# Kernel tuning notes

Measured on AMD Instinct MI355X. Metric: run time of the kernel, lower is better.

## Reference

```python
import jax, jax.numpy as jnp
import numpy as np

PROJ = 8192     # projDim
THRESH = 1e-8   # numerical-stability epsilon for signed sqrt
L2_EPS = 1e-12  # eps of torch F.normalize


def setup_inputs() -> dict:
    key = jax.random.key(0)
    k1, k2, k3, k4, k5 = jax.random.split(key, 5)
    B, C, H, W = 16, 512, 14, 14
    x = jax.random.normal(k1, (B, C, H, W), dtype=jnp.float32)
    h1 = jax.random.randint(k2, (C,), 0, PROJ, dtype=jnp.int32)
    h2 = jax.random.randint(k3, (C,), 0, PROJ, dtype=jnp.int32)
    s1 = (2 * jax.random.randint(k4, (C,), 0, 2) - 1).astype(jnp.float32)
    s2 = (2 * jax.random.randint(k5, (C,), 0, 2) - 1).astype(jnp.float32)
    return {"x": x, "s1": s1, "s2": s2, "h1": h1, "h2": h2}


def reference(x, s1, s2, h1, h2):
    # x: [B, C, H, W]; h*: [C] hash buckets in [0, PROJ); s*: [C] signs (+-1)
    B, C, H, W = x.shape
    x_flat = jnp.transpose(x, (0, 2, 3, 1)).reshape(-1, C)  # [N, C], N = B*H*W

    def count_sketch(s, h):
        # Equivalent to x_flat @ M with M[c, h[c]] = s[c]: scatter-add of
        # sign-weighted channels into PROJ bins.  -> [N, PROJ]
        return jax.ops.segment_sum((x_flat * s).T, h, num_segments=PROJ).T

    fft1 = jnp.fft.fft(count_sketch(s1, h1), axis=-1)
    fft2 = jnp.fft.fft(count_sketch(s2, h2), axis=-1)
    conv = jnp.fft.ifft(fft1 * fft2, axis=-1).real       # [N, PROJ]
    y = conv.reshape(B, H, W, PROJ).sum(axis=(1, 2))      # sum pool -> [B, PROJ]
    y = jnp.sign(y) * jnp.sqrt(jnp.abs(y) + THRESH)       # signed sqrt
    norm = jnp.linalg.norm(y, axis=1, keepdims=True)
    return y / jnp.maximum(norm, L2_EPS)                  # l2 normalize (dim=1)
```

## Files before the change

### kernel.cpp

```cpp
#include <hip/hip_runtime.h>
#include <math.h>

#define PROJ 8192
#define NB   16
#define NC   512
#define HW   196
#define NKC  7
#define LST  40

typedef __attribute__((ext_vector_type(8))) short bf16x8;
typedef __attribute__((ext_vector_type(4))) short short4v;
typedef __attribute__((ext_vector_type(4))) float f32x4;

__device__ __forceinline__ unsigned bf16_rne(float f) {
    unsigned u = __builtin_bit_cast(unsigned, f);
    return (u + 0x7fffu + ((u >> 16) & 1u)) >> 16;
}

__global__ __launch_bounds__(1024, 4)
void cbp_gram_mfma(const float* __restrict__ x,
                   const float* __restrict__ s1,
                   const float* __restrict__ s2,
                   const int*   __restrict__ h1,
                   const int*   __restrict__ h2,
                   float* __restrict__ gsk) {
    __shared__ float sk[PROJ];
    __shared__ short Ah[128 * LST];
    __shared__ short Al[128 * LST];
    __shared__ short Bh[128 * LST];
    __shared__ short Bl[128 * LST];
    __shared__ int   lh1[128], lh2[128];
    __shared__ float lsA[128], lsB[128];

    const int tid = threadIdx.x;
    const int blk = blockIdx.x;
    const int b    = 2 * (blk & 7) + (blk >> 7);
    const int tile = (blk >> 3) & 15;
    const int I = tile >> 2, J = tile & 3;
    const int c1base = I * 128;
    const int c2base = J * 128;

    const int lane = tid & 63;
    const int wave = tid >> 6;
    const int quad = lane >> 4;
    const int l15  = lane & 15;
    const int wr   = (wave >> 2) * 32;
    const int wc   = (wave & 3) * 32;

    for (int i = tid; i < PROJ; i += 1024) sk[i] = 0.f;
    if (tid < 128) {
        lh1[tid] = h1[c1base + tid];  lsA[tid] = s1[c1base + tid];
        lh2[tid] = h2[c2base + tid];  lsB[tid] = s2[c2base + tid];
    }

    const float* xa = x + ((size_t)b * NC + c1base) * HW;
    const float* xb = x + ((size_t)b * NC + c2base) * HW;

    f32x4 acc[2][2];
#pragma unroll
    for (int i = 0; i < 2; ++i)
#pragma unroll
        for (int j = 0; j < 2; ++j) acc[i][j] = (f32x4){0.f, 0.f, 0.f, 0.f};

    const int sr0 = tid >> 3;
    const int sq  = tid & 7;

    float4 pa, pb;
    {
        const int kk = 4 * sq;
        const bool ok = (kk + 3 < HW);
        pa = ok ? *(const float4*)&xa[sr0 * HW + kk] : (float4){0.f,0.f,0.f,0.f};
        pb = ok ? *(const float4*)&xb[sr0 * HW + kk] : (float4){0.f,0.f,0.f,0.f};
    }

    for (int kc = 0; kc < NKC; ++kc) {
        __syncthreads();
        {
            const float sA = lsA[sr0], sB = lsB[sr0];
            const float fa[4] = {pa.x*sA, pa.y*sA, pa.z*sA, pa.w*sA};
            const float fb[4] = {pb.x*sB, pb.y*sB, pb.z*sB, pb.w*sB};
            short4v ah, al, bh, bl;
#pragma unroll
            for (int c = 0; c < 4; ++c) {
                const unsigned ha_ = bf16_rne(fa[c]);
                ah[c] = (short)ha_;
                al[c] = (short)bf16_rne(fa[c] - __builtin_bit_cast(float, ha_ << 16));
                const unsigned hb_ = bf16_rne(fb[c]);
                bh[c] = (short)hb_;
                bl[c] = (short)bf16_rne(fb[c] - __builtin_bit_cast(float, hb_ << 16));
            }
            *(short4v*)&Ah[sr0 * LST + 4 * sq] = ah;
            *(short4v*)&Al[sr0 * LST + 4 * sq] = al;
            *(short4v*)&Bh[sr0 * LST + 4 * sq] = bh;
            *(short4v*)&Bl[sr0 * LST + 4 * sq] = bl;
        }
        if (kc + 1 < NKC) {
            const int kk = (kc + 1) * 32 + 4 * sq;
            const bool ok = (kk + 3 < HW);
            pa = ok ? *(const float4*)&xa[sr0 * HW + kk] : (float4){0.f,0.f,0.f,0.f};
            pb = ok ? *(const float4*)&xb[sr0 * HW + kk] : (float4){0.f,0.f,0.f,0.f};
        }
        __syncthreads();

        bf16x8 ahf[2], alf[2], bhf[2], blf[2];
#pragma unroll
        for (int i = 0; i < 2; ++i) {
            const int ra = wr + i * 16 + l15;
            ahf[i] = *(const bf16x8*)&Ah[ra * LST + quad * 8];
            alf[i] = *(const bf16x8*)&Al[ra * LST + quad * 8];
        }
#pragma unroll
        for (int j = 0; j < 2; ++j) {
            const int rb = wc + j * 16 + l15;
            bhf[j] = *(const bf16x8*)&Bh[rb * LST + quad * 8];
            blf[j] = *(const bf16x8*)&Bl[rb * LST + quad * 8];
        }
#pragma unroll
        for (int i = 0; i < 2; ++i)
#pragma unroll
            for (int j = 0; j < 2; ++j) {
                acc[i][j] = __builtin_amdgcn_mfma_f32_16x16x32_bf16(ahf[i], bhf[j], acc[i][j], 0, 0, 0);
                acc[i][j] = __builtin_amdgcn_mfma_f32_16x16x32_bf16(ahf[i], blf[j], acc[i][j], 0, 0, 0);
                acc[i][j] = __builtin_amdgcn_mfma_f32_16x16x32_bf16(alf[i], bhf[j], acc[i][j], 0, 0, 0);
            }
    }
    __syncthreads();

#pragma unroll
    for (int i = 0; i < 2; ++i) {
        const int lr0 = wr + i * 16 + quad * 4;
#pragma unroll
        for (int j = 0; j < 2; ++j) {
            const int h2v = lh2[wc + j * 16 + l15];
#pragma unroll
            for (int rg = 0; rg < 4; ++rg) {
                const int bin = (lh1[lr0 + rg] + h2v) & (PROJ - 1);
                atomicAdd(&sk[bin], acc[i][j][rg]);
            }
        }
    }
    __syncthreads();

    float* gs = gsk + (size_t)b * PROJ;
    for (int i = tid; i < PROJ; i += 1024) atomicAdd(&gs[i], sk[i]);
}

__device__ __forceinline__ float ssqrt(float s) {
    const float m = sqrtf(fabsf(s) + 1e-8f);
    return (s > 0.f) ? m : (s < 0.f ? -m : 0.f);
}

__global__ __launch_bounds__(512)
void cbp_finalize(const float* __restrict__ gsk, float* __restrict__ y) {
    __shared__ float red[8];
    const int b   = blockIdx.x;
    const int tid = threadIdx.x;
    const float4* gp = (const float4*)(gsk + (size_t)b * PROJ);

    float4 ov[4];
    float ssq = 0.f;
#pragma unroll
    for (int g = 0; g < 4; ++g) {
        const float4 s = gp[tid + 512 * g];
        float4 o;
        o.x = ssqrt(s.x); o.y = ssqrt(s.y); o.z = ssqrt(s.z); o.w = ssqrt(s.w);
        ov[g] = o;
        ssq += o.x * o.x + o.y * o.y + o.z * o.z + o.w * o.w;
    }

    float v = ssq;
#pragma unroll
    for (int off = 32; off >= 1; off >>= 1) v += __shfl_xor(v, off, 64);
    if ((tid & 63) == 0) red[tid >> 6] = v;
    __syncthreads();
    float tot = 0.f;
#pragma unroll
    for (int w = 0; w < 8; ++w) tot += red[w];
    const float inv = 1.0f / fmaxf(sqrtf(tot), 1e-12f);

    float4* yp = (float4*)(y + (size_t)b * PROJ);
#pragma unroll
    for (int g = 0; g < 4; ++g) {
        float4 o = ov[g];
        o.x *= inv; o.y *= inv; o.z *= inv; o.w *= inv;
        yp[tid + 512 * g] = o;
    }
}

extern "C" void kernel_launch(void* const* d_in, const int* in_sizes, int n_in,
                              void* d_out, int out_size, void* d_ws, size_t ws_size,
                              hipStream_t stream) {
    const float* x  = (const float*)d_in[0];
    const float* s1 = (const float*)d_in[1];
    const float* s2 = (const float*)d_in[2];
    const int*   h1 = (const int*)d_in[3];
    const int*   h2 = (const int*)d_in[4];
    float* y   = (float*)d_out;
    float* gsk = (float*)d_ws;

    hipMemsetAsync(gsk, 0, (size_t)NB * PROJ * sizeof(float), stream);
    hipLaunchKernelGGL(cbp_gram_mfma, dim3(256), dim3(1024), 0, stream,
                       x, s1, s2, h1, h2, gsk);
    hipLaunchKernelGGL(cbp_finalize, dim3(16), dim3(512), 0, stream, gsk, y);
}
```

Baseline: 103.9 us.

## Prefetch all K-chunks of x into registers before the MFMA loop

Issues all seven float4 global loads per operand up front, converts them to hi/lo bf16 pairs in registers, and only then runs the LDS-stage/MFMA loop. This replaces the one-chunk-ahead prefetch so global memory latency is exposed once instead of per iteration. Sign values are now read straight from global memory rather than staged through shared arrays. Register pressure rises (28 short4 values plus 14 float4 temporaries) at 1024 threads with launch bounds of 4 blocks, which risks spills or lower occupancy.

```diff
diff --git a/kernel.cpp b/kernel.cpp
--- a/kernel.cpp
+++ b/kernel.cpp
@@ -30,7 +30,6 @@
     __shared__ short Bh[128 * LST];
     __shared__ short Bl[128 * LST];
     __shared__ int   lh1[128], lh2[128];
-    __shared__ float lsA[128], lsB[128];
 
     const int tid = threadIdx.x;
     const int blk = blockIdx.x;
@@ -48,37 +47,31 @@
     const int wc   = (wave & 3) * 32;
 
     for (int i = tid; i < PROJ; i += 1024) sk[i] = 0.f;
-    if (tid < 128) {
-        lh1[tid] = h1[c1base + tid];  lsA[tid] = s1[c1base + tid];
-        lh2[tid] = h2[c2base + tid];  lsB[tid] = s2[c2base + tid];
-    }
-
-    const float* xa = x + ((size_t)b * NC + c1base) * HW;
-    const float* xb = x + ((size_t)b * NC + c2base) * HW;
-
-    f32x4 acc[2][2];
-#pragma unroll
-    for (int i = 0; i < 2; ++i)
-#pragma unroll
-        for (int j = 0; j < 2; ++j) acc[i][j] = (f32x4){0.f, 0.f, 0.f, 0.f};
+    if (tid < 128) { lh1[tid] = h1[c1base + tid]; lh2[tid] = h2[c2base + tid]; }
 
     const int sr0 = tid >> 3;
     const int sq  = tid & 7;
 
-    float4 pa, pb;
+    const float* xa = x + ((size_t)b * NC + c1base) * HW + sr0 * HW;
+    const float* xb = x + ((size_t)b * NC + c2base) * HW + sr0 * HW;
+    const float sA = s1[c1base + sr0];
+    const float sB = s2[c2base + sr0];
+
+    short4v cah[NKC], cal[NKC], cbh[NKC], cbl[NKC];
     {
-        const int kk = 4 * sq;
-        const bool ok = (kk + 3 < HW);
-        pa = ok ? *(const float4*)&xa[sr0 * HW + kk] : (float4){0.f,0.f,0.f,0.f};
-        pb = ok ? *(const float4*)&xb[sr0 * HW + kk] : (float4){0.f,0.f,0.f,0.f};
-    }
-
-    for (int kc = 0; kc < NKC; ++kc) {
-        __syncthreads();
-        {
-            const float sA = lsA[sr0], sB = lsB[sr0];
-            const float fa[4] = {pa.x*sA, pa.y*sA, pa.z*sA, pa.w*sA};
-            const float fb[4] = {pb.x*sB, pb.y*sB, pb.z*sB, pb.w*sB};
+        const float4 z4 = {0.f, 0.f, 0.f, 0.f};
+        float4 pa[NKC], pb[NKC];
+#pragma unroll
+        for (int kc = 0; kc < NKC; ++kc) {
+            const int kk = kc * 32 + 4 * sq;
+            const bool ok = (kk + 3 < HW);
+            pa[kc] = ok ? *(const float4*)&xa[kk] : z4;
+            pb[kc] = ok ? *(const float4*)&xb[kk] : z4;
+        }
+#pragma unroll
+        for (int kc = 0; kc < NKC; ++kc) {
+            const float fa[4] = {pa[kc].x*sA, pa[kc].y*sA, pa[kc].z*sA, pa[kc].w*sA};
+            const float fb[4] = {pb[kc].x*sB, pb[kc].y*sB, pb[kc].z*sB, pb[kc].w*sB};
             short4v ah, al, bh, bl;
 #pragma unroll
             for (int c = 0; c < 4; ++c) {
@@ -89,17 +82,23 @@
                 bh[c] = (short)hb_;
                 bl[c] = (short)bf16_rne(fb[c] - __builtin_bit_cast(float, hb_ << 16));
             }
-            *(short4v*)&Ah[sr0 * LST + 4 * sq] = ah;
-            *(short4v*)&Al[sr0 * LST + 4 * sq] = al;
-            *(short4v*)&Bh[sr0 * LST + 4 * sq] = bh;
-            *(short4v*)&Bl[sr0 * LST + 4 * sq] = bl;
-        }
-        if (kc + 1 < NKC) {
-            const int kk = (kc + 1) * 32 + 4 * sq;
-            const bool ok = (kk + 3 < HW);
-            pa = ok ? *(const float4*)&xa[sr0 * HW + kk] : (float4){0.f,0.f,0.f,0.f};
-            pb = ok ? *(const float4*)&xb[sr0 * HW + kk] : (float4){0.f,0.f,0.f,0.f};
-        }
+            cah[kc] = ah; cal[kc] = al; cbh[kc] = bh; cbl[kc] = bl;
+        }
+    }
+
+    f32x4 acc[2][2];
+#pragma unroll
+    for (int i = 0; i < 2; ++i)
+#pragma unroll
+        for (int j = 0; j < 2; ++j) acc[i][j] = (f32x4){0.f, 0.f, 0.f, 0.f};
+
+#pragma unroll
+    for (int kc = 0; kc < NKC; ++kc) {
+        __syncthreads();
+        *(short4v*)&Ah[sr0 * LST + 4 * sq] = cah[kc];
+        *(short4v*)&Al[sr0 * LST + 4 * sq] = cal[kc];
+        *(short4v*)&Bh[sr0 * LST + 4 * sq] = cbh[kc];
+        *(short4v*)&Bl[sr0 * LST + 4 * sq] = cbl[kc];
         __syncthreads();
 
         bf16x8 ahf[2], alf[2], bhf[2], blf[2];
```

After: 104.5 us. Within noise of the previous version (+0.6%).
